# Kernel optimization log

Measured on AMD Instinct MI355X. Metric: run time of the kernel, lower is better.

Reference implementation:

```python
import jax, jax.numpy as jnp
import numpy as np

SLOPE = 15.0

@jax.custom_vjp
def spike_fn(x):
    return (x > 0).astype(x.dtype)

def _spike_fwd(x):
    return (x > 0).astype(x.dtype), x

def _spike_bwd(x, g):
    # fast_sigmoid surrogate: d/dx = 1 / (slope*|x| + 1)^2
    return (g / (SLOPE * jnp.abs(x) + 1.0) ** 2,)

spike_fn.defvjp(_spike_fwd, _spike_bwd)

def setup_inputs() -> dict:
    key = jax.random.key(0)
    ks = jax.random.split(key, 8)
    B, T, C = 256, 500, 700
    x = jax.random.uniform(ks[0], (B, T, C), dtype=jnp.float32)
    def lin(k, fan_in, fan_out):
        kw, kb = jax.random.split(k)
        bound = 1.0 / np.sqrt(fan_in)
        W = jax.random.uniform(kw, (fan_out, fan_in), minval=-bound, maxval=bound, dtype=jnp.float32)
        b = jax.random.uniform(kb, (fan_out,), minval=-bound, maxval=bound, dtype=jnp.float32)
        return W, b
    W1, b1 = lin(ks[1], C, 128)
    W2, b2 = lin(ks[2], 128, 256)
    W3, b3 = lin(ks[3], 256, 20)
    beta = jnp.float32(0.8)
    thr = jnp.float32(1.0)
    return {"x": x, "W1": W1, "b1": b1, "W2": W2, "b2": b2, "W3": W3, "b3": b3,
            "beta1": beta, "beta2": beta, "beta3": beta,
            "thr1": thr, "thr2": thr, "thr3": thr}

def _lif(mem, cur, beta, thr):
    # snntorch Leaky, reset_mechanism='subtract': reset from previous mem (detached)
    reset = jax.lax.stop_gradient((mem - thr > 0).astype(mem.dtype))
    mem = jnp.clip(beta, 0.0, 1.0) * mem + cur - reset * thr
    spk = spike_fn(mem - thr)
    return spk, mem

def reference(x, W1, b1, W2, b2, W3, b3, beta1, beta2, beta3, thr1, thr2, thr3):
    B, T, C = x.shape
    xt = jnp.swapaxes(x, 0, 1)  # [T, B, C]

    def step(carry, x_t):
        m1, m2, m3 = carry
        cur1 = x_t @ W1.T + b1
        s1, m1 = _lif(m1, cur1, beta1, thr1)
        cur2 = s1 @ W2.T + b2
        s2, m2 = _lif(m2, cur2, beta2, thr2)
        cur3 = s2 @ W3.T + b3
        s3, m3 = _lif(m3, cur3, beta3, thr3)
        return (m1, m2, m3), s3

    init = (jnp.zeros((B, 128), x.dtype), jnp.zeros((B, 256), x.dtype), jnp.zeros((B, 20), x.dtype))
    _, spk3 = jax.lax.scan(step, init, xt)  # [T, B, 20]
    return spk3.mean(axis=0)  # [B, 20]
```

## Files before the change

kernel.cpp:

```cpp
#include <hip/hip_runtime.h>

typedef __attribute__((ext_vector_type(8))) short short8;
typedef __attribute__((ext_vector_type(4))) float f32x4;

#define MFMA16(a, b, c) __builtin_amdgcn_mfma_f32_16x16x32_bf16(a, b, c, 0, 0, 0)

__device__ __forceinline__ ushort bf16_rne(float f) {
  uint u = __float_as_uint(f);
  u += 0x7FFFu + ((u >> 16) & 1u);
  return (ushort)(u >> 16);
}

__device__ __forceinline__ void gload_lds16(const void* g, void* l) {
  __builtin_amdgcn_global_load_lds((const __attribute__((address_space(1))) uint*)g,
                                   (__attribute__((address_space(3))) uint*)l, 16, 0, 0);
}

__global__ void split_w_kernel(const float* __restrict__ W, ushort* __restrict__ hi,
                               ushort* __restrict__ lo, int Nr, int K, int Npad, int Kp) {
  int i = blockIdx.x * 256 + threadIdx.x;
  if (i >= Npad * Kp) return;
  int r = i / Kp, k = i - r * Kp;
  float v = (r < Nr && k < K) ? W[(size_t)r * K + k] : 0.f;
  ushort h = bf16_rne(v);
  float hf = __uint_as_float(((uint)h) << 16);
  ushort l = bf16_rne(v - hf);
  hi[i] = h;
  lo[i] = l;
}

__global__ __launch_bounds__(256, 3) void gemm1_kernel(const float* __restrict__ A,
                                                       const ushort* __restrict__ Bh,
                                                       const ushort* __restrict__ Bl,
                                                       float* __restrict__ C) {
  __shared__ ushort sAh[64 * 64];
  __shared__ ushort sAl[64 * 64];
  __shared__ ushort sBh[128 * 64];
  __shared__ ushort sBl[128 * 64];

  const int tid = threadIdx.x;
  const int lane = tid & 63;
  const int wid = tid >> 6;
  const int tr = tid >> 2, tg = tid & 3;
  const int wr = wid >> 1, wc = wid & 1;
  const int m0 = blockIdx.x * 64;

  const int brow_lo = lane >> 3;
  const int bswz = (((lane & 7) ^ brow_lo) << 3);
  const size_t bgoff = (size_t)(wid * 32 + brow_lo) * 704 + bswz;

  f32x4 acc[2][4];
#pragma unroll
  for (int i = 0; i < 2; ++i)
#pragma unroll
    for (int j = 0; j < 4; ++j) acc[i][j] = f32x4{0.f, 0.f, 0.f, 0.f};

  float4 pf[4];
  auto load_a = [&](int ks) {
    const float* ap = A + (size_t)(m0 + tr) * 700 + ks * 64 + tg * 16;
#pragma unroll
    for (int q = 0; q < 4; ++q) {
      float4 z;
      z.x = z.y = z.z = z.w = 0.f;
      pf[q] = (ks * 64 + tg * 16 + q * 4 + 3 < 700) ? *(const float4*)(ap + q * 4) : z;
    }
  };
  load_a(0);

  for (int ks = 0; ks < 11; ++ks) {
#pragma unroll
    for (int p = 0; p < 4; ++p) {
      const size_t go = bgoff + (size_t)p * 8 * 704 + ks * 64;
      gload_lds16(Bh + go, &sBh[(wid * 32 + p * 8) * 64]);
      gload_lds16(Bl + go, &sBl[(wid * 32 + p * 8) * 64]);
    }
#pragma unroll
    for (int h = 0; h < 2; ++h) {
      const float* vf = (const float*)&pf[h * 2];
      uint hw[4], lw[4];
#pragma unroll
      for (int q = 0; q < 4; ++q) {
        const uint u0 = __float_as_uint(vf[2 * q]);
        const uint u1 = __float_as_uint(vf[2 * q + 1]);
        hw[q] = __builtin_amdgcn_perm(u1, u0, 0x07060302u);
        const float d0 = vf[2 * q] - __uint_as_float(u0 & 0xFFFF0000u);
        const float d1 = vf[2 * q + 1] - __uint_as_float(u1 & 0xFFFF0000u);
        asm("v_cvt_pk_bf16_f32 %0, %1, %2" : "=v"(lw[q]) : "v"(d0), "v"(d1));
      }
      const int off = tr * 64 + (((tg * 2 + h) ^ (tr & 7)) << 3);
      uint4 qh, ql;
      qh.x = hw[0]; qh.y = hw[1]; qh.z = hw[2]; qh.w = hw[3];
      ql.x = lw[0]; ql.y = lw[1]; ql.z = lw[2]; ql.w = lw[3];
      *(uint4*)&sAh[off] = qh;
      *(uint4*)&sAl[off] = ql;
    }
    __syncthreads();
    if (ks < 10) load_a(ks + 1);

#pragma unroll
    for (int ku = 0; ku < 2; ++ku) {
      const int g0 = ku * 4 + (lane >> 4);
      short8 ah[2], al[2];
#pragma unroll
      for (int i = 0; i < 2; ++i) {
        const int r = wr * 32 + i * 16 + (lane & 15);
        const int off = r * 64 + ((g0 ^ (r & 7)) << 3);
        ah[i] = *(const short8*)&sAh[off];
        al[i] = *(const short8*)&sAl[off];
      }
      short8 bh[4], bl[4];
#pragma unroll
      for (int j = 0; j < 4; ++j) {
        const int r = wc * 64 + j * 16 + (lane & 15);
        const int off = r * 64 + ((g0 ^ (r & 7)) << 3);
        bh[j] = *(const short8*)&sBh[off];
        bl[j] = *(const short8*)&sBl[off];
      }
#pragma unroll
      for (int i = 0; i < 2; ++i)
#pragma unroll
        for (int j = 0; j < 4; ++j) {
          acc[i][j] = MFMA16(ah[i], bh[j], acc[i][j]);
          acc[i][j] = MFMA16(al[i], bh[j], acc[i][j]);
          acc[i][j] = MFMA16(ah[i], bl[j], acc[i][j]);
        }
    }
    __syncthreads();
  }

#pragma unroll
  for (int i = 0; i < 2; ++i) {
    const int rbase = m0 + wr * 32 + i * 16 + ((lane >> 4) << 2);
#pragma unroll
    for (int j = 0; j < 4; ++j) {
      const int col = wc * 64 + j * 16 + (lane & 15);
#pragma unroll
      for (int rg = 0; rg < 4; ++rg)
        C[(size_t)(rbase + rg) * 128 + col] = acc[i][j][rg];
    }
  }
}

__global__ __launch_bounds__(512, 1) void fused_l23_kernel(
    const float* __restrict__ cur1, const float* __restrict__ b1,
    const ushort* __restrict__ w2h, const ushort* __restrict__ w2l, const float* __restrict__ b2,
    const ushort* __restrict__ w3h, const ushort* __restrict__ w3l, const float* __restrict__ b3,
    const float* __restrict__ beta1p, const float* __restrict__ beta2p,
    const float* __restrict__ beta3p, const float* __restrict__ thr1p,
    const float* __restrict__ thr2p, const float* __restrict__ thr3p,
    float* __restrict__ out) {
  __shared__ __align__(16) char smem[147456];
  float* buf = (float*)smem;
  ushort* s2 = (ushort*)smem;
  ushort* s1 = (ushort*)(smem + 32768);
  float* c3 = (float*)(smem + 32768);
  ushort* stage = (ushort*)(smem + 49152);
  float* c2 = (float*)(smem + 49152);
  ushort* w3p = (ushort*)(smem + 114688);

  const int tid = threadIdx.x;
  const int lane = tid & 63;
  const int w = tid >> 6;
  const int b = blockIdx.x;
  const int tg8 = tid & 7, wrow = tid >> 3;

  const float be1 = fminf(fmaxf(beta1p[0], 0.f), 1.f), th1 = thr1p[0];
  const float be2 = fminf(fmaxf(beta2p[0], 0.f), 1.f), th2 = thr2p[0];
  const float be3 = fminf(fmaxf(beta3p[0], 0.f), 1.f), th3 = thr3p[0];
  const float bi1 = (tid < 128) ? b1[tid] : 0.f;
  const float bi2 = (tid < 256) ? b2[tid] : 0.f;
  const float bi3 = (tid < 20) ? b3[tid] : 0.f;

#pragma unroll
  for (int p = 0; p < 2; ++p) {
    const int r = p * 16 + (tid >> 5);
    const int g = tid & 31;
    const int swz = ((g ^ (r & 7)) << 3);
    *(uint4*)&w3p[r * 256 + g * 8] = *(const uint4*)(w3h + r * 256 + swz);
    *(uint4*)&w3p[8192 + r * 256 + g * 8] = *(const uint4*)(w3l + r * 256 + swz);
  }
  const float4* cg4 = (const float4*)cur1 + (size_t)b * 16000;
#pragma unroll
  for (int i = 0; i < 4; ++i) ((float4*)buf)[i * 512 + tid] = cg4[i * 512 + tid];
  __syncthreads();

  float m1 = 0.f, m2 = 0.f, m3 = 0.f, a3 = 0.f;

  for (int c = 0; c < 8; ++c) {
    const int t0 = c * 64;

    if (tid < 128) {
      const int g = tid >> 3, nb = tid & 7;
#pragma unroll
      for (int hh = 0; hh < 2; ++hh) {
        float v[32];
#pragma unroll
        for (int u = 0; u < 32; ++u) v[u] = buf[(hh * 32 + u) * 128 + tid];
#pragma unroll
        for (int u = 0; u < 32; ++u) {
          const int row = hh * 32 + u;
          const int t = t0 + row;
          ushort sp = 0;
          if (t < 500) {
            float r = (m1 > th1) ? th1 : 0.f;
            m1 = be1 * m1 + (v[u] + bi1) - r;
            sp = (m1 > th1) ? (ushort)0x3F80 : (ushort)0;
          }
          s1[row * 128 + ((g ^ (row & 7)) << 3) + nb] = sp;
        }
      }
    }
    __syncthreads();

    f32x4 acc[4][2];
#pragma unroll
    for (int i = 0; i < 4; ++i)
#pragma unroll
      for (int j = 0; j < 2; ++j) acc[i][j] = f32x4{0.f, 0.f, 0.f, 0.f};

#pragma unroll
    for (int kst = 0; kst < 2; ++kst) {
#pragma unroll
      for (int p = 0; p < 4; ++p) {
        const int r = p * 64 + wrow;
        const int off2 = r * 64 + ((tg8 ^ (r & 7)) << 3);
        *(uint4*)&stage[off2] = *(const uint4*)(w2h + r * 128 + kst * 64 + tg8 * 8);
        *(uint4*)&stage[16384 + off2] = *(const uint4*)(w2l + r * 128 + kst * 64 + tg8 * 8);
      }
      short8 ah[2][4];
#pragma unroll
      for (int ku = 0; ku < 2; ++ku) {
        const int G = kst * 8 + ku * 4 + (lane >> 4);
#pragma unroll
        for (int i = 0; i < 4; ++i) {
          const int r = i * 16 + (lane & 15);
          ah[ku][i] = *(const short8*)&s1[r * 128 + ((G ^ (r & 7)) << 3)];
        }
      }
      __syncthreads();
#pragma unroll
      for (int ku = 0; ku < 2; ++ku) {
        const int gB = ku * 4 + (lane >> 4);
#pragma unroll
        for (int j = 0; j < 2; ++j) {
          const int rb = w * 32 + j * 16 + (lane & 15);
          const int off = rb * 64 + ((gB ^ (rb & 7)) << 3);
          short8 bh = *(const short8*)&stage[off];
          short8 bl = *(const short8*)&stage[16384 + off];
#pragma unroll
          for (int i = 0; i < 4; ++i) {
            acc[i][j] = MFMA16(ah[ku][i], bh, acc[i][j]);
            acc[i][j] = MFMA16(ah[ku][i], bl, acc[i][j]);
          }
        }
      }
      __syncthreads();
    }
#pragma unroll
    for (int i = 0; i < 4; ++i) {
      const int rbase = i * 16 + ((lane >> 4) << 2);
#pragma unroll
      for (int j = 0; j < 2; ++j) {
        const int col = w * 32 + j * 16 + (lane & 15);
#pragma unroll
        for (int rg = 0; rg < 4; ++rg) {
          const int row = rbase + rg;
          c2[row * 256 + (col ^ ((row & 7) << 2))] = acc[i][j][rg];
        }
      }
    }
    __syncthreads();

    if (tid < 256) {
      const int g = tid >> 3, nb = tid & 7;
#pragma unroll
      for (int hh = 0; hh < 2; ++hh) {
        float v[32];
#pragma unroll
        for (int u = 0; u < 32; ++u) {
          const int row = hh * 32 + u;
          v[u] = c2[row * 256 + (tid ^ ((row & 7) << 2))];
        }
#pragma unroll
        for (int u = 0; u < 32; ++u) {
          const int row = hh * 32 + u;
          const int t = t0 + row;
          ushort sp = 0;
          if (t < 500) {
            float r = (m2 > th2) ? th2 : 0.f;
            m2 = be2 * m2 + (v[u] + bi2) - r;
            sp = (m2 > th2) ? (ushort)0x3F80 : (ushort)0;
          }
          s2[row * 256 + ((g ^ (row & 7)) << 3) + nb] = sp;
        }
      }
    }
    __syncthreads();

    {
      const int wr3 = w >> 1, wc3 = w & 1;
      f32x4 a3c = f32x4{0.f, 0.f, 0.f, 0.f};
#pragma unroll
      for (int ku = 0; ku < 8; ++ku) {
        const int G = ku * 4 + (lane >> 4);
        const int rb = wc3 * 16 + (lane & 15);
        const int ob = rb * 256 + ((G ^ (rb & 7)) << 3);
        short8 vbh = *(const short8*)&w3p[ob];
        short8 vbl = *(const short8*)&w3p[8192 + ob];
        const int r = wr3 * 16 + (lane & 15);
        short8 av = *(const short8*)&s2[r * 256 + ((G ^ (r & 7)) << 3)];
        a3c = MFMA16(av, vbh, a3c);
        a3c = MFMA16(av, vbl, a3c);
      }
      const int rb3 = wr3 * 16 + ((lane >> 4) << 2);
      const int col3 = wc3 * 16 + (lane & 15);
#pragma unroll
      for (int rg = 0; rg < 4; ++rg) c3[(rb3 + rg) * 36 + col3] = a3c[rg];
    }
    __syncthreads();

    if (tid < 20) {
#pragma unroll 8
      for (int u = 0; u < 64; ++u) {
        const int t = t0 + u;
        if (t < 500) {
          const float v = c3[u * 36 + tid];
          float r = (m3 > th3) ? th3 : 0.f;
          m3 = be3 * m3 + (v + bi3) - r;
          a3 += (m3 > th3) ? 1.f : 0.f;
        }
      }
    } else if (tid >= 64 && c < 7) {
      const int base = (c + 1) * 2048;
#pragma unroll
      for (int i = 0; i < 5; ++i) {
        const int idx = i * 448 + (tid - 64);
        if (idx < 2048) ((float4*)buf)[idx] = cg4[base + idx];
      }
    }
    __syncthreads();
  }
  if (tid < 20) out[(size_t)b * 20 + tid] = a3 * (1.f / 500.f);
}

extern "C" void kernel_launch(void* const* d_in, const int* in_sizes, int n_in, void* d_out,
                              int out_size, void* d_ws, size_t ws_size, hipStream_t stream) {
  const float* x = (const float*)d_in[0];
  const float* W1 = (const float*)d_in[1];
  const float* b1 = (const float*)d_in[2];
  const float* W2 = (const float*)d_in[3];
  const float* b2 = (const float*)d_in[4];
  const float* W3 = (const float*)d_in[5];
  const float* b3 = (const float*)d_in[6];
  const float* beta1 = (const float*)d_in[7];
  const float* beta2 = (const float*)d_in[8];
  const float* beta3 = (const float*)d_in[9];
  const float* thr1 = (const float*)d_in[10];
  const float* thr2 = (const float*)d_in[11];
  const float* thr3 = (const float*)d_in[12];
  float* out = (float*)d_out;

  const int M = 128000;
  char* ws = (char*)d_ws;
  float* cur1 = (float*)ws;
  size_t off = (size_t)M * 128 * 4;
  ushort* w1h = (ushort*)(ws + off); off += 128 * 704 * 2;
  ushort* w1l = (ushort*)(ws + off); off += 128 * 704 * 2;
  ushort* w2h = (ushort*)(ws + off); off += 256 * 128 * 2;
  ushort* w2l = (ushort*)(ws + off); off += 256 * 128 * 2;
  ushort* w3h = (ushort*)(ws + off); off += 32 * 256 * 2;
  ushort* w3l = (ushort*)(ws + off); off += 32 * 256 * 2;

  split_w_kernel<<<(128 * 704 + 255) / 256, 256, 0, stream>>>(W1, w1h, w1l, 128, 700, 128, 704);
  split_w_kernel<<<(256 * 128 + 255) / 256, 256, 0, stream>>>(W2, w2h, w2l, 256, 128, 256, 128);
  split_w_kernel<<<(32 * 256 + 255) / 256, 256, 0, stream>>>(W3, w3h, w3l, 20, 256, 32, 256);

  gemm1_kernel<<<M / 64, 256, 0, stream>>>(x, w1h, w1l, cur1);
  fused_l23_kernel<<<256, 512, 0, stream>>>(cur1, b1, w2h, w2l, b2, w3h, w3l, b3,
                                            beta1, beta2, beta3, thr1, thr2, thr3, out);
}
```

Before: 224.8 us.

## Load GEMM1 operands directly from global into registers, dropping LDS staging

The layer-1 GEMM no longer stages A and B tiles through shared memory with barriers. Each wave now reads its own A rows and B fragments from global memory straight into MFMA register layout, doing the bf16 hi/lo split in registers. The K tail is peeled into a separate masked iteration, and occupancy is lowered from 3 to 2 blocks per CU. This removes LDS traffic and synchronisation, but A and B are now re-read by multiple waves through cache, with no explicit prefetch to hide global latency.

```diff
diff --git a/kernel.cpp b/kernel.cpp
--- a/kernel.cpp
+++ b/kernel.cpp
@@ -9,11 +9,6 @@
   uint u = __float_as_uint(f);
   u += 0x7FFFu + ((u >> 16) & 1u);
   return (ushort)(u >> 16);
-}
-
-__device__ __forceinline__ void gload_lds16(const void* g, void* l) {
-  __builtin_amdgcn_global_load_lds((const __attribute__((address_space(1))) uint*)g,
-                                   (__attribute__((address_space(3))) uint*)l, 16, 0, 0);
 }
 
 __global__ void split_w_kernel(const float* __restrict__ W, ushort* __restrict__ hi,
@@ -29,25 +24,33 @@
   lo[i] = l;
 }
 
-__global__ __launch_bounds__(256, 3) void gemm1_kernel(const float* __restrict__ A,
+__device__ __forceinline__ void cvt8(const float4 f0, const float4 f1, short8& hi8, short8& lo8) {
+  const float vf[8] = {f0.x, f0.y, f0.z, f0.w, f1.x, f1.y, f1.z, f1.w};
+  union { uint u[4]; short8 s; } H, L;
+#pragma unroll
+  for (int q = 0; q < 4; ++q) {
+    const uint u0 = __float_as_uint(vf[2 * q]);
+    const uint u1 = __float_as_uint(vf[2 * q + 1]);
+    H.u[q] = __builtin_amdgcn_perm(u1, u0, 0x07060302u);
+    const float d0 = vf[2 * q] - __uint_as_float(u0 & 0xFFFF0000u);
+    const float d1 = vf[2 * q + 1] - __uint_as_float(u1 & 0xFFFF0000u);
+    asm("v_cvt_pk_bf16_f32 %0, %1, %2" : "=v"(L.u[q]) : "v"(d0), "v"(d1));
+  }
+  hi8 = H.s;
+  lo8 = L.s;
+}
+
+__global__ __launch_bounds__(256, 2) void gemm1_kernel(const float* __restrict__ A,
                                                        const ushort* __restrict__ Bh,
                                                        const ushort* __restrict__ Bl,
                                                        float* __restrict__ C) {
-  __shared__ ushort sAh[64 * 64];
-  __shared__ ushort sAl[64 * 64];
-  __shared__ ushort sBh[128 * 64];
-  __shared__ ushort sBl[128 * 64];
-
   const int tid = threadIdx.x;
   const int lane = tid & 63;
   const int wid = tid >> 6;
-  const int tr = tid >> 2, tg = tid & 3;
   const int wr = wid >> 1, wc = wid & 1;
   const int m0 = blockIdx.x * 64;
-
-  const int brow_lo = lane >> 3;
-  const int bswz = (((lane & 7) ^ brow_lo) << 3);
-  const size_t bgoff = (size_t)(wid * 32 + brow_lo) * 704 + bswz;
+  const int lr = lane & 15;
+  const int lg = lane >> 4;
 
   f32x4 acc[2][4];
 #pragma unroll
@@ -55,77 +58,72 @@
 #pragma unroll
     for (int j = 0; j < 4; ++j) acc[i][j] = f32x4{0.f, 0.f, 0.f, 0.f};
 
-  float4 pf[4];
-  auto load_a = [&](int ks) {
-    const float* ap = A + (size_t)(m0 + tr) * 700 + ks * 64 + tg * 16;
-#pragma unroll
-    for (int q = 0; q < 4; ++q) {
-      float4 z;
-      z.x = z.y = z.z = z.w = 0.f;
-      pf[q] = (ks * 64 + tg * 16 + q * 4 + 3 < 700) ? *(const float4*)(ap + q * 4) : z;
-    }
-  };
-  load_a(0);
-
-  for (int ks = 0; ks < 11; ++ks) {
-#pragma unroll
-    for (int p = 0; p < 4; ++p) {
-      const size_t go = bgoff + (size_t)p * 8 * 704 + ks * 64;
-      gload_lds16(Bh + go, &sBh[(wid * 32 + p * 8) * 64]);
-      gload_lds16(Bl + go, &sBl[(wid * 32 + p * 8) * 64]);
-    }
-#pragma unroll
-    for (int h = 0; h < 2; ++h) {
-      const float* vf = (const float*)&pf[h * 2];
-      uint hw[4], lw[4];
-#pragma unroll
-      for (int q = 0; q < 4; ++q) {
-        const uint u0 = __float_as_uint(vf[2 * q]);
-        const uint u1 = __float_as_uint(vf[2 * q + 1]);
-        hw[q] = __builtin_amdgcn_perm(u1, u0, 0x07060302u);
-        const float d0 = vf[2 * q] - __uint_as_float(u0 & 0xFFFF0000u);
-        const float d1 = vf[2 * q + 1] - __uint_as_float(u1 & 0xFFFF0000u);
-        asm("v_cvt_pk_bf16_f32 %0, %1, %2" : "=v"(lw[q]) : "v"(d0), "v"(d1));
-      }
-      const int off = tr * 64 + (((tg * 2 + h) ^ (tr & 7)) << 3);
-      uint4 qh, ql;
-      qh.x = hw[0]; qh.y = hw[1]; qh.z = hw[2]; qh.w = hw[3];
-      ql.x = lw[0]; ql.y = lw[1]; ql.z = lw[2]; ql.w = lw[3];
-      *(uint4*)&sAh[off] = qh;
-      *(uint4*)&sAl[off] = ql;
-    }
-    __syncthreads();
-    if (ks < 10) load_a(ks + 1);
-
+  const float* arow0 = A + (size_t)(m0 + wr * 32 + lr) * 700 + lg * 8;
+  const float* arow1 = arow0 + (size_t)16 * 700;
+  const ushort* bbase[4];
+#pragma unroll
+  for (int j = 0; j < 4; ++j)
+    bbase[j] = Bh + (size_t)(wc * 64 + j * 16 + lr) * 704 + lg * 8;
+  const ptrdiff_t lo_off = Bl - Bh;
+
+  for (int ks = 0; ks < 10; ++ks) {
+    const int k0 = ks * 64;
+    short8 ah[2][2], al[2][2];
 #pragma unroll
     for (int ku = 0; ku < 2; ++ku) {
-      const int g0 = ku * 4 + (lane >> 4);
-      short8 ah[2], al[2];
-#pragma unroll
-      for (int i = 0; i < 2; ++i) {
-        const int r = wr * 32 + i * 16 + (lane & 15);
-        const int off = r * 64 + ((g0 ^ (r & 7)) << 3);
-        ah[i] = *(const short8*)&sAh[off];
-        al[i] = *(const short8*)&sAl[off];
-      }
-      short8 bh[4], bl[4];
+      const float* a0 = arow0 + k0 + ku * 32;
+      const float* a1 = arow1 + k0 + ku * 32;
+      cvt8(*(const float4*)a0, *(const float4*)(a0 + 4), ah[0][ku], al[0][ku]);
+      cvt8(*(const float4*)a1, *(const float4*)(a1 + 4), ah[1][ku], al[1][ku]);
+    }
+#pragma unroll
+    for (int ku = 0; ku < 2; ++ku) {
 #pragma unroll
       for (int j = 0; j < 4; ++j) {
-        const int r = wc * 64 + j * 16 + (lane & 15);
-        const int off = r * 64 + ((g0 ^ (r & 7)) << 3);
-        bh[j] = *(const short8*)&sBh[off];
-        bl[j] = *(const short8*)&sBl[off];
-      }
-#pragma unroll
-      for (int i = 0; i < 2; ++i)
-#pragma unroll
-        for (int j = 0; j < 4; ++j) {
-          acc[i][j] = MFMA16(ah[i], bh[j], acc[i][j]);
-          acc[i][j] = MFMA16(al[i], bh[j], acc[i][j]);
-          acc[i][j] = MFMA16(ah[i], bl[j], acc[i][j]);
-        }
-    }
-    __syncthreads();
+        const ushort* bp = bbase[j] + k0 + ku * 32;
+        const short8 bh = *(const short8*)bp;
+        const short8 bl = *(const short8*)(bp + lo_off);
+#pragma unroll
+        for (int i = 0; i < 2; ++i) {
+          acc[i][j] = MFMA16(ah[i][ku], bh, acc[i][j]);
+          acc[i][j] = MFMA16(al[i][ku], bh, acc[i][j]);
+          acc[i][j] = MFMA16(ah[i][ku], bl, acc[i][j]);
+        }
+      }
+    }
+  }
+
+  {
+    const int k0 = 640;
+    const float4 z = {0.f, 0.f, 0.f, 0.f};
+    short8 ah[2][2], al[2][2];
+#pragma unroll
+    for (int ku = 0; ku < 2; ++ku) {
+      const int kb = k0 + ku * 32 + lg * 8;
+      const float* a0 = arow0 + k0 + ku * 32;
+      const float* a1 = arow1 + k0 + ku * 32;
+      const float4 f00 = (kb + 3 < 700) ? *(const float4*)a0 : z;
+      const float4 f01 = (kb + 7 < 700) ? *(const float4*)(a0 + 4) : z;
+      const float4 f10 = (kb + 3 < 700) ? *(const float4*)a1 : z;
+      const float4 f11 = (kb + 7 < 700) ? *(const float4*)(a1 + 4) : z;
+      cvt8(f00, f01, ah[0][ku], al[0][ku]);
+      cvt8(f10, f11, ah[1][ku], al[1][ku]);
+    }
+#pragma unroll
+    for (int ku = 0; ku < 2; ++ku) {
+#pragma unroll
+      for (int j = 0; j < 4; ++j) {
+        const ushort* bp = bbase[j] + k0 + ku * 32;
+        const short8 bh = *(const short8*)bp;
+        const short8 bl = *(const short8*)(bp + lo_off);
+#pragma unroll
+        for (int i = 0; i < 2; ++i) {
+          acc[i][j] = MFMA16(ah[i][ku], bh, acc[i][j]);
+          acc[i][j] = MFMA16(al[i][ku], bh, acc[i][j]);
+          acc[i][j] = MFMA16(ah[i][ku], bl, acc[i][j]);
+        }
+      }
+    }
   }
 
 #pragma unroll
```

Result: slower. 351.6 us (+56.5%).

## Keep W2 fragments in registers and overlap layer-3 LIF with next chunk

Applied to the files above, without the earlier changes.

Each wave now loads its slice of the bf16 hi/lo W2 fragments into registers once at kernel start, so the per-chunk LDS staging of W2 and the extra barriers around it go away. The layer-3 LIF scan for chunk c-1 is deferred and runs on threads 128-147 alongside the layer-1 scan of chunk c, with c3 moved to its own LDS region. The prefetch of the next cur1 chunk now runs on the upper 256 threads while the lower 256 read c2, and launch bounds change to 2 blocks per CU. The cost is more registers per thread and a larger shared-memory footprint, which may conflict with the occupancy hint.

```diff
diff --git a/kernel.cpp b/kernel.cpp
--- a/kernel.cpp
+++ b/kernel.cpp
@@ -141,7 +141,7 @@
   }
 }
 
-__global__ __launch_bounds__(512, 1) void fused_l23_kernel(
+__global__ __launch_bounds__(512, 2) void fused_l23_kernel(
     const float* __restrict__ cur1, const float* __restrict__ b1,
     const ushort* __restrict__ w2h, const ushort* __restrict__ w2l, const float* __restrict__ b2,
     const ushort* __restrict__ w3h, const ushort* __restrict__ w3l, const float* __restrict__ b3,
@@ -149,28 +149,36 @@
     const float* __restrict__ beta3p, const float* __restrict__ thr1p,
     const float* __restrict__ thr2p, const float* __restrict__ thr3p,
     float* __restrict__ out) {
-  __shared__ __align__(16) char smem[147456];
+  __shared__ __align__(16) char smem[156672];
   float* buf = (float*)smem;
-  ushort* s2 = (ushort*)smem;
   ushort* s1 = (ushort*)(smem + 32768);
-  float* c3 = (float*)(smem + 32768);
-  ushort* stage = (ushort*)(smem + 49152);
   float* c2 = (float*)(smem + 49152);
+  ushort* s2 = (ushort*)(smem + 49152);
   ushort* w3p = (ushort*)(smem + 114688);
+  float* c3 = (float*)(smem + 147456);
 
   const int tid = threadIdx.x;
   const int lane = tid & 63;
   const int w = tid >> 6;
   const int b = blockIdx.x;
-  const int tg8 = tid & 7, wrow = tid >> 3;
+  const int lr = lane & 15, lg = lane >> 4;
 
   const float be1 = fminf(fmaxf(beta1p[0], 0.f), 1.f), th1 = thr1p[0];
   const float be2 = fminf(fmaxf(beta2p[0], 0.f), 1.f), th2 = thr2p[0];
   const float be3 = fminf(fmaxf(beta3p[0], 0.f), 1.f), th3 = thr3p[0];
   const float bi1 = (tid < 128) ? b1[tid] : 0.f;
   const float bi2 = (tid < 256) ? b2[tid] : 0.f;
-  const float bi3 = (tid < 20) ? b3[tid] : 0.f;
-
+  const float bi3 = (tid >= 128 && tid < 148) ? b3[tid - 128] : 0.f;
+
+  short8 w2fh[2][4], w2fl[2][4];
+#pragma unroll
+  for (int j = 0; j < 2; ++j)
+#pragma unroll
+    for (int ks = 0; ks < 4; ++ks) {
+      const size_t o = (size_t)(w * 32 + j * 16 + lr) * 128 + ks * 32 + lg * 8;
+      w2fh[j][ks] = *(const short8*)(w2h + o);
+      w2fl[j][ks] = *(const short8*)(w2l + o);
+    }
 #pragma unroll
   for (int p = 0; p < 2; ++p) {
     const int r = p * 16 + (tid >> 5);
@@ -209,90 +217,98 @@
           s1[row * 128 + ((g ^ (row & 7)) << 3) + nb] = sp;
         }
       }
-    }
-    __syncthreads();
-
-    f32x4 acc[4][2];
-#pragma unroll
-    for (int i = 0; i < 4; ++i)
-#pragma unroll
-      for (int j = 0; j < 2; ++j) acc[i][j] = f32x4{0.f, 0.f, 0.f, 0.f};
-
-#pragma unroll
-    for (int kst = 0; kst < 2; ++kst) {
-#pragma unroll
-      for (int p = 0; p < 4; ++p) {
-        const int r = p * 64 + wrow;
-        const int off2 = r * 64 + ((tg8 ^ (r & 7)) << 3);
-        *(uint4*)&stage[off2] = *(const uint4*)(w2h + r * 128 + kst * 64 + tg8 * 8);
-        *(uint4*)&stage[16384 + off2] = *(const uint4*)(w2l + r * 128 + kst * 64 + tg8 * 8);
-      }
-      short8 ah[2][4];
-#pragma unroll
-      for (int ku = 0; ku < 2; ++ku) {
-        const int G = kst * 8 + ku * 4 + (lane >> 4);
+    } else if (tid < 148 && c > 0) {
+      const int n = tid - 128;
+      const int tp = (c - 1) * 64;
+#pragma unroll 8
+      for (int u = 0; u < 64; ++u) {
+        if (tp + u < 500) {
+          const float v = c3[u * 36 + n];
+          float r = (m3 > th3) ? th3 : 0.f;
+          m3 = be3 * m3 + (v + bi3) - r;
+          a3 += (m3 > th3) ? 1.f : 0.f;
+        }
+      }
+    }
+    __syncthreads();
+
+    {
+      f32x4 acc[4][2];
+#pragma unroll
+      for (int i = 0; i < 4; ++i)
+#pragma unroll
+        for (int j = 0; j < 2; ++j) acc[i][j] = f32x4{0.f, 0.f, 0.f, 0.f};
+#pragma unroll
+      for (int ks = 0; ks < 4; ++ks) {
+        const int G = ks * 4 + lg;
+        short8 ah[4];
 #pragma unroll
         for (int i = 0; i < 4; ++i) {
-          const int r = i * 16 + (lane & 15);
-          ah[ku][i] = *(const short8*)&s1[r * 128 + ((G ^ (r & 7)) << 3)];
-        }
-      }
-      __syncthreads();
-#pragma unroll
-      for (int ku = 0; ku < 2; ++ku) {
-        const int gB = ku * 4 + (lane >> 4);
+          const int r = i * 16 + lr;
+          ah[i] = *(const short8*)&s1[r * 128 + ((G ^ (r & 7)) << 3)];
+        }
+#pragma unroll
+        for (int j = 0; j < 2; ++j)
+#pragma unroll
+          for (int i = 0; i < 4; ++i) {
+            acc[i][j] = MFMA16(ah[i], w2fh[j][ks], acc[i][j]);
+            acc[i][j] = MFMA16(ah[i], w2fl[j][ks], acc[i][j]);
+          }
+      }
+#pragma unroll
+      for (int i = 0; i < 4; ++i) {
+        const int rbase = i * 16 + (lg << 2);
 #pragma unroll
         for (int j = 0; j < 2; ++j) {
-          const int rb = w * 32 + j * 16 + (lane & 15);
-          const int off = rb * 64 + ((gB ^ (rb & 7)) << 3);
-          short8 bh = *(const short8*)&stage[off];
-          short8 bl = *(const short8*)&stage[16384 + off];
-#pragma unroll
-          for (int i = 0; i < 4; ++i) {
-            acc[i][j] = MFMA16(ah[ku][i], bh, acc[i][j]);
-            acc[i][j] = MFMA16(ah[ku][i], bl, acc[i][j]);
+          const int col = w * 32 + j * 16 + lr;
+#pragma unroll
+          for (int rg = 0; rg < 4; ++rg) {
+            const int row = rbase + rg;
+            c2[row * 256 + (col ^ ((row & 7) << 2))] = acc[i][j][rg];
           }
         }
       }
-      __syncthreads();
-    }
-#pragma unroll
-    for (int i = 0; i < 4; ++i) {
-      const int rbase = i * 16 + ((lane >> 4) << 2);
-#pragma unroll
-      for (int j = 0; j < 2; ++j) {
-        const int col = w * 32 + j * 16 + (lane & 15);
-#pragma unroll
-        for (int rg = 0; rg < 4; ++rg) {
-          const int row = rbase + rg;
-          c2[row * 256 + (col ^ ((row & 7) << 2))] = acc[i][j][rg];
-        }
-      }
+    }
+    __syncthreads();
+
+    float v[32];
+    if (tid < 256) {
+#pragma unroll
+      for (int u = 0; u < 32; ++u) v[u] = c2[u * 256 + (tid ^ ((u & 7) << 2))];
+    } else if (c < 7) {
+      const int base = (c + 1) * 2048;
+#pragma unroll
+      for (int i = 0; i < 8; ++i)
+        ((float4*)buf)[i * 256 + (tid - 256)] = cg4[base + i * 256 + (tid - 256)];
     }
     __syncthreads();
 
     if (tid < 256) {
       const int g = tid >> 3, nb = tid & 7;
 #pragma unroll
-      for (int hh = 0; hh < 2; ++hh) {
-        float v[32];
-#pragma unroll
-        for (int u = 0; u < 32; ++u) {
-          const int row = hh * 32 + u;
-          v[u] = c2[row * 256 + (tid ^ ((row & 7) << 2))];
-        }
-#pragma unroll
-        for (int u = 0; u < 32; ++u) {
-          const int row = hh * 32 + u;
-          const int t = t0 + row;
-          ushort sp = 0;
-          if (t < 500) {
-            float r = (m2 > th2) ? th2 : 0.f;
-            m2 = be2 * m2 + (v[u] + bi2) - r;
-            sp = (m2 > th2) ? (ushort)0x3F80 : (ushort)0;
-          }
-          s2[row * 256 + ((g ^ (row & 7)) << 3) + nb] = sp;
-        }
+      for (int u = 0; u < 32; ++u) {
+        const int t = t0 + u;
+        ushort sp = 0;
+        if (t < 500) {
+          float r = (m2 > th2) ? th2 : 0.f;
+          m2 = be2 * m2 + (v[u] + bi2) - r;
+          sp = (m2 > th2) ? (ushort)0x3F80 : (ushort)0;
+        }
+        s2[u * 256 + ((g ^ (u & 7)) << 3) + nb] = sp;
+      }
+#pragma unroll
+      for (int u = 0; u < 32; ++u) v[u] = c2[(32 + u) * 256 + (tid ^ ((u & 7) << 2))];
+#pragma unroll
+      for (int u = 0; u < 32; ++u) {
+        const int row = 32 + u;
+        const int t = t0 + row;
+        ushort sp = 0;
+        if (t < 500) {
+          float r = (m2 > th2) ? th2 : 0.f;
+          m2 = be2 * m2 + (v[u] + bi2) - r;
+          sp = (m2 > th2) ? (ushort)0x3F80 : (ushort)0;
+        }
+        s2[row * 256 + ((g ^ (row & 7)) << 3) + nb] = sp;
       }
     }
     __syncthreads();
@@ -302,45 +318,37 @@
       f32x4 a3c = f32x4{0.f, 0.f, 0.f, 0.f};
 #pragma unroll
       for (int ku = 0; ku < 8; ++ku) {
-        const int G = ku * 4 + (lane >> 4);
-        const int rb = wc3 * 16 + (lane & 15);
+        const int G = ku * 4 + lg;
+        const int rb = wc3 * 16 + lr;
         const int ob = rb * 256 + ((G ^ (rb & 7)) << 3);
         short8 vbh = *(const short8*)&w3p[ob];
         short8 vbl = *(const short8*)&w3p[8192 + ob];
-        const int r = wr3 * 16 + (lane & 15);
+        const int r = wr3 * 16 + lr;
         short8 av = *(const short8*)&s2[r * 256 + ((G ^ (r & 7)) << 3)];
         a3c = MFMA16(av, vbh, a3c);
         a3c = MFMA16(av, vbl, a3c);
       }
-      const int rb3 = wr3 * 16 + ((lane >> 4) << 2);
-      const int col3 = wc3 * 16 + (lane & 15);
+      const int rb3 = wr3 * 16 + (lg << 2);
+      const int col3 = wc3 * 16 + lr;
 #pragma unroll
       for (int rg = 0; rg < 4; ++rg) c3[(rb3 + rg) * 36 + col3] = a3c[rg];
     }
     __syncthreads();
-
-    if (tid < 20) {
+  }
+
+  if (tid >= 128 && tid < 148) {
+    const int n = tid - 128;
 #pragma unroll 8
-      for (int u = 0; u < 64; ++u) {
-        const int t = t0 + u;
-        if (t < 500) {
-          const float v = c3[u * 36 + tid];
-          float r = (m3 > th3) ? th3 : 0.f;
-          m3 = be3 * m3 + (v + bi3) - r;
-          a3 += (m3 > th3) ? 1.f : 0.f;
-        }
-      }
-    } else if (tid >= 64 && c < 7) {
-      const int base = (c + 1) * 2048;
-#pragma unroll
-      for (int i = 0; i < 5; ++i) {
-        const int idx = i * 448 + (tid - 64);
-        if (idx < 2048) ((float4*)buf)[idx] = cg4[base + idx];
-      }
-    }
-    __syncthreads();
-  }
-  if (tid < 20) out[(size_t)b * 20 + tid] = a3 * (1.f / 500.f);
+    for (int u = 0; u < 64; ++u) {
+      if (448 + u < 500) {
+        const float v = c3[u * 36 + n];
+        float r = (m3 > th3) ? th3 : 0.f;
+        m3 = be3 * m3 + (v + bi3) - r;
+        a3 += (m3 > th3) ? 1.f : 0.f;
+      }
+    }
+    out[(size_t)b * 20 + n] = a3 * (1.f / 500.f);
+  }
 }
 
 extern "C" void kernel_launch(void* const* d_in, const int* in_sizes, int n_in, void* d_out,
```

After: 188.7 us (median of 2 runs). -16.1%, faster.
